# Performance work log

Measured on AMD Instinct MI355X. Metric: run time of the kernel, lower is better.

The kernel has to match this reference:

```python
import jax, jax.numpy as jnp
import numpy as np

EPS = 1e-4


def softmax_kernel(data, projection, is_query):
    # data: [b,h,n,d]; projection: [F,d]
    d = data.shape[-1]
    data_normalizer = d ** -0.25
    ratio = projection.shape[0] ** -0.5
    # [b,h,n,F]
    data_dash = jnp.einsum('bhnd,fd->bhnf', data_normalizer * data, projection)
    diag_data = (0.5 * (data_normalizer ** 2)) * jnp.sum(data * data, axis=-1, keepdims=True)
    if is_query:
        stab = jnp.max(data_dash, axis=-1, keepdims=True)
    else:
        stab = jnp.max(data_dash)
    return ratio * (jnp.exp(data_dash - diag_data - stab) + EPS)


def linear_attention(q, k, v):
    # q,k: [b,h,n,F]; v: [b,h,n,e]
    k_sum = k.sum(axis=-2)                                   # [b,h,F]
    d_inv = 1.0 / jnp.einsum('bhnf,bhf->bhn', q, k_sum)      # [b,h,n]
    context = jnp.einsum('bhnf,bhne->bhfe', k, v)            # [b,h,F,e]
    return jnp.einsum('bhfe,bhnf,bhn->bhne', context, q, d_inv)


def _gaussian_orthogonal_random_matrix(nb_rows, nb_cols, seed=0):
    # scaling=0: rows are orthogonal blocks rescaled by norms of iid gaussian rows
    rng = np.random.default_rng(seed)
    blocks = []
    full_blocks = nb_rows // nb_cols
    for _ in range(full_blocks):
        g = rng.standard_normal((nb_cols, nb_cols))
        qm, _ = np.linalg.qr(g)
        blocks.append(qm.T)
    rem = nb_rows - full_blocks * nb_cols
    if rem > 0:
        g = rng.standard_normal((nb_cols, nb_cols))
        qm, _ = np.linalg.qr(g)
        blocks.append(qm.T[:rem])
    mat = np.concatenate(blocks, axis=0)
    multiplier = np.linalg.norm(rng.standard_normal((nb_rows, nb_cols)), axis=1)
    return (multiplier[:, None] * mat).astype(np.float32)


def setup_inputs() -> dict:
    key = jax.random.key(0)
    kq, kk, kv = jax.random.split(key, 3)
    B, H, N, D = 2, 8, 8192, 64
    F = 256  # nb_features
    q = jax.random.normal(kq, (B, H, N, D), dtype=jnp.float32)
    k = jax.random.normal(kk, (B, H, N, D), dtype=jnp.float32)
    v = jax.random.normal(kv, (B, H, N, D), dtype=jnp.float32)
    projection = jnp.asarray(_gaussian_orthogonal_random_matrix(F, D, seed=0))
    return {"q": q, "k": k, "v": v, "projection": projection}


def reference(q, k, v, projection):
    qp = softmax_kernel(q, projection, is_query=True)
    kp = softmax_kernel(k, projection, is_query=False)
    return linear_attention(qp, kp, v)
```

## Files before the change

kernel.cpp:

```cpp
#include <hip/hip_runtime.h>


typedef __bf16 bf16;
typedef __bf16 bf16x8 __attribute__((ext_vector_type(8)));
typedef _Float16 f16;
typedef f16 f16x8 __attribute__((ext_vector_type(8)));
typedef float f32x4 __attribute__((ext_vector_type(4)));

#define N_    8192
#define BH_   16
#define NRM   0.35355339059327379f
#define RATIO 0.0625f
#define DSC   0.0625f
#define REPS  6.25e-6f

#define CTX_W  16
#define KSUM_W (CTX_W + BH_*256*64)
#define ZERO_W (KSUM_W + BH_*256)
#define SLICE_W 16640
#define PART_W  ZERO_W

static __device__ __forceinline__ unsigned mapmax(float x){
  unsigned u=__float_as_uint(x); return (u&0x80000000u)? ~u : (u|0x80000000u);
}
static __device__ __forceinline__ float unmapmax(unsigned u){
  return __uint_as_float((u&0x80000000u)? (u&0x7fffffffu) : ~u);
}
static __device__ __forceinline__ f32x4 mfma16(bf16x8 a, bf16x8 b, f32x4 c){
  return __builtin_amdgcn_mfma_f32_16x16x32_bf16(a,b,c,0,0,0);
}
static __device__ __forceinline__ f32x4 mfma16h(f16x8 a, f16x8 b, f32x4 c){
  return __builtin_amdgcn_mfma_f32_16x16x32_f16(a,b,c,0,0,0);
}
static __device__ __forceinline__ void ld8(const float* __restrict__ p, float* x){
  float4 a=*(const float4*)p; float4 b=*(const float4*)(p+4);
  x[0]=a.x; x[1]=a.y; x[2]=a.z; x[3]=a.w; x[4]=b.x; x[5]=b.y; x[6]=b.z; x[7]=b.w;
}
static __device__ __forceinline__ void split8(const float* x, bf16x8& h, bf16x8& l){
  #pragma unroll
  for(int i=0;i<8;++i){ bf16 hi=(bf16)x[i]; h[i]=hi; l[i]=(bf16)(x[i]-(float)hi); }
}
static __device__ __forceinline__ void cvt8b(const float* x, bf16x8& h){
  #pragma unroll
  for(int i=0;i<8;++i) h[i]=(bf16)x[i];
}
static __device__ __forceinline__ void cvt8h(const float* x, f16x8& h){
  #pragma unroll
  for(int i=0;i<8;++i) h[i]=(f16)x[i];
}
static __device__ __forceinline__ void gload16(const float* g, float* l){
  __builtin_amdgcn_global_load_lds(
      (const __attribute__((address_space(1))) unsigned*)g,
      (__attribute__((address_space(3))) unsigned*)l, 16, 0, 0);
}
static __device__ __forceinline__ void load_P_frags1(const float* __restrict__ Pg,
    int fb, int l15, int g, bf16x8 (&pb)[4][2]){
  #pragma unroll
  for(int ft=0;ft<4;++ft)
    #pragma unroll
    for(int ks=0;ks<2;++ks){
      float x[8]; ld8(&Pg[(fb+16*ft+l15)*64+32*ks+8*g],x);
      #pragma unroll
      for(int i=0;i<8;++i) x[i]*=NRM;
      cvt8b(x,pb[ft][ks]);
    }
}

#define STAGE32(Xg, bufptr, n0s) do{                                      \
    int u0_=tid, u1_=tid+256;                                             \
    int r0_=u0_>>4, c0_=u0_&15, r1_=u1_>>4, c1_=u1_&15;                   \
    gload16((Xg)+((n0s)+r0_)*64+((c0_^(r0_&15))<<2), (bufptr)+u0_*4);     \
    gload16((Xg)+((n0s)+r1_)*64+((c1_^(r1_&15))<<2), (bufptr)+u1_*4);     \
  }while(0)
#define STAGE64(Xg, bufptr, n0s) do{                                      \
    _Pragma("unroll")                                                     \
    for(int ii_=0;ii_<4;++ii_){                                           \
      int u_=tid+256*ii_;                                                 \
      int r_=u_>>4, c_=u_&15;                                             \
      gload16((Xg)+((n0s)+r_)*64+((c_^(r_&15))<<2), (bufptr)+u_*4);       \
    }                                                                     \
  }while(0)
#define FRAGREAD(xv, bufptr, rr, ksv) do{                                 \
    int cc0_=(8*(ksv)+2*g)^((rr)&15);                                     \
    int cc1_=cc0_^1;                                                      \
    float4 a_=*(const float4*)((bufptr)+(rr)*64+cc0_*4);                  \
    float4 b_=*(const float4*)((bufptr)+(rr)*64+cc1_*4);                  \
    xv[0]=a_.x; xv[1]=a_.y; xv[2]=a_.z; xv[3]=a_.w;                       \
    xv[4]=b_.x; xv[5]=b_.y; xv[6]=b_.z; xv[7]=b_.w;                       \
  }while(0)


__global__ void __launch_bounds__(256) initK(unsigned* ws, int n){
  for(int i=blockIdx.x*256+threadIdx.x;i<n;i+=gridDim.x*256) ws[i]=0u;
}

__global__ void __launch_bounds__(256) stabK(const float* __restrict__ Kg,
                                             const float* __restrict__ Pg,
                                             unsigned* __restrict__ stab_ws){
  __shared__ float red[4];
  int tid=threadIdx.x, w=tid>>6, lane=tid&63, l15=lane&15, g=lane>>4;
  int fb=w*64;
  f16x8 pb[4][2];
  #pragma unroll
  for(int ft=0;ft<4;++ft)
    #pragma unroll
    for(int ks=0;ks<2;++ks){
      float x[8]; ld8(&Pg[(fb+16*ft+l15)*64+32*ks+8*g],x);
      #pragma unroll
      for(int i=0;i<8;++i) x[i]*=NRM;
      cvt8h(x,pb[ft][ks]);
    }
  float m=-3.4e38f;
  long base=(long)blockIdx.x*512;
  f32x4 zero={0.f,0.f,0.f,0.f};
  #pragma unroll 1
  for(int it=0;it<8;++it){
    long row0=base+it*64;
    f16x8 ka[4][2];
    #pragma unroll
    for(int rt=0;rt<4;++rt)
      #pragma unroll
      for(int ks=0;ks<2;++ks){
        float x[8]; ld8(&Kg[(row0+16*rt+l15)*64+32*ks+8*g],x);
        cvt8h(x,ka[rt][ks]);
      }
    f32x4 acc[4][4];
    #pragma unroll
    for(int rt=0;rt<4;++rt)
      #pragma unroll
      for(int ft=0;ft<4;++ft) acc[rt][ft]=zero;
    __builtin_amdgcn_s_setprio(1);
    #pragma unroll
    for(int rt=0;rt<4;++rt)
      #pragma unroll
      for(int ft=0;ft<4;++ft)
        #pragma unroll
        for(int ks=0;ks<2;++ks)
          acc[rt][ft]=mfma16h(ka[rt][ks],pb[ft][ks],acc[rt][ft]);
    __builtin_amdgcn_s_setprio(0);
    #pragma unroll
    for(int rt=0;rt<4;++rt)
      #pragma unroll
      for(int ft=0;ft<4;++ft)
        #pragma unroll
        for(int r=0;r<4;++r) m=fmaxf(m,acc[rt][ft][r]);
  }
  #pragma unroll
  for(int off=1;off<64;off<<=1) m=fmaxf(m,__shfl_xor(m,off));
  if(lane==0) red[w]=m;
  __syncthreads();
  if(tid==0){
    m=fmaxf(fmaxf(red[0],red[1]),fmaxf(red[2],red[3]));
    atomicMax(stab_ws,mapmax(m));
  }
}

__global__ void __launch_bounds__(256,2) ctxK(const float* __restrict__ Kg,
    const float* __restrict__ Vg, const float* __restrict__ Pg,
    const unsigned* __restrict__ stab_ws, float* __restrict__ ctx_g,
    float* __restrict__ ksum_g, float* __restrict__ part, int mode){
  __shared__ __align__(16) bf16 kpt_h[256*40];
  __shared__ float kstage[2][2048];
  int tid=threadIdx.x, w=tid>>6, lane=tid&63, l15=lane&15, g=lane>>4;
  int fb=w*64;
  int bh=blockIdx.x>>5, ch=blockIdx.x&31;
  long rowbase=(long)bh*N_ + ch*256;
  float stab=unmapmax(*stab_ws);
  bf16x8 pb[4][2];
  load_P_frags1(Pg,fb,l15,g,pb);
  f32x4 zero={0.f,0.f,0.f,0.f};
  f32x4 cacc[4][4];
  #pragma unroll
  for(int mt=0;mt<4;++mt)
    #pragma unroll
    for(int et=0;et<4;++et) cacc[mt][et]=zero;
  float ksacc[4]={0.f,0.f,0.f,0.f};
  int cur=0;
  STAGE32(Kg, &kstage[0][0], rowbase);
  __syncthreads();
  #pragma unroll 1
  for(int it=0;it<8;++it){
    long n0=rowbase+it*32;
    long np=(it==7)? rowbase : n0+32;
    STAGE32(Kg, &kstage[cur^1][0], np);
    float vx[4][8];
    #pragma unroll
    for(int et=0;et<4;++et)
      #pragma unroll
      for(int j=0;j<8;++j) vx[et][j]=Vg[(n0+8*g+j)*64+16*et+l15];
    bf16x8 ka[2][2];
    float dsq[2];
    #pragma unroll
    for(int rt=0;rt<2;++rt){
      float ss=0.f;
      #pragma unroll
      for(int ks=0;ks<2;++ks){
        float x[8]; FRAGREAD(x,&kstage[cur][0],16*rt+l15,ks);
        #pragma unroll
        for(int i=0;i<8;++i) ss=fmaf(x[i],x[i],ss);
        cvt8b(x,ka[rt][ks]);
      }
      ss+=__shfl_xor(ss,16); ss+=__shfl_xor(ss,32);
      dsq[rt]=DSC*ss;
    }
    f32x4 dacc[2][4];
    #pragma unroll
    for(int rt=0;rt<2;++rt)
      #pragma unroll
      for(int ft=0;ft<4;++ft) dacc[rt][ft]=zero;
    __builtin_amdgcn_s_setprio(1);
    #pragma unroll
    for(int rt=0;rt<2;++rt)
      #pragma unroll
      for(int ft=0;ft<4;++ft)
        #pragma unroll
        for(int ks=0;ks<2;++ks)
          dacc[rt][ft]=mfma16(ka[rt][ks],pb[ft][ks],dacc[rt][ft]);
    __builtin_amdgcn_s_setprio(0);
    float dg[2][4];
    #pragma unroll
    for(int rt=0;rt<2;++rt)
      #pragma unroll
      for(int r=0;r<4;++r) dg[rt][r]=__shfl(dsq[rt],4*g+r);
    #pragma unroll
    for(int rt=0;rt<2;++rt)
      #pragma unroll
      for(int ft=0;ft<4;++ft){
        int f=fb+16*ft+l15;
        ushort4 pk;
        unsigned short hvb[4];
        #pragma unroll
        for(int r=0;r<4;++r){
          float kp=fmaf(RATIO,__expf(dacc[rt][ft][r]-dg[rt][r]-stab),REPS);
          bf16 hb=(bf16)kp;
          ksacc[ft]+=(float)hb;
          hvb[r]=__builtin_bit_cast(unsigned short,hb);
        }
        pk.x=hvb[0]; pk.y=hvb[1]; pk.z=hvb[2]; pk.w=hvb[3];
        *(ushort4*)&kpt_h[f*40+16*rt+4*g]=pk;
      }
    bf16x8 vb_h[4], vb_l[4];
    #pragma unroll
    for(int et=0;et<4;++et) split8(vx[et],vb_h[et],vb_l[et]);
    __builtin_amdgcn_s_setprio(1);
    #pragma unroll
    for(int mt=0;mt<4;++mt){
      bf16x8 a_h=*(const bf16x8*)&kpt_h[(fb+16*mt+l15)*40+8*g];
      #pragma unroll
      for(int et=0;et<4;++et){
        cacc[mt][et]=mfma16(a_h,vb_h[et],cacc[mt][et]);
        cacc[mt][et]=mfma16(a_h,vb_l[et],cacc[mt][et]);
      }
    }
    __builtin_amdgcn_s_setprio(0);
    __syncthreads();
    cur^=1;
  }
  float ksred[4];
  #pragma unroll
  for(int ft=0;ft<4;++ft){
    float s=ksacc[ft];
    s+=__shfl_xor(s,16); s+=__shfl_xor(s,32);
    ksred[ft]=s;
  }
  if(mode){
    float* cg=part+((long)ch*BH_+bh)*SLICE_W;
    #pragma unroll
    for(int mt=0;mt<4;++mt)
      #pragma unroll
      for(int et=0;et<4;++et)
        #pragma unroll
        for(int r=0;r<4;++r)
          cg[(fb+16*mt+4*g+r)*64+16*et+l15]=cacc[mt][et][r];
    if(g==0){
      #pragma unroll
      for(int ft=0;ft<4;++ft)
        cg[16384+fb+16*ft+l15]=ksred[ft];
    }
  }else{
    float* cg=ctx_g+(long)bh*16384;
    #pragma unroll
    for(int mt=0;mt<4;++mt)
      #pragma unroll
      for(int et=0;et<4;++et)
        #pragma unroll
        for(int r=0;r<4;++r)
          atomicAdd(&cg[(fb+16*mt+4*g+r)*64+16*et+l15],cacc[mt][et][r]);
    if(g==0){
      #pragma unroll
      for(int ft=0;ft<4;++ft)
        atomicAdd(&ksum_g[bh*256+fb+16*ft+l15],ksred[ft]);
    }
  }
}

__global__ void __launch_bounds__(256) redK(const float* __restrict__ part,
    float* __restrict__ ctx_g, float* __restrict__ ksum_g){
  const long TOT4=(long)BH_*(SLICE_W/4);
  long t=(long)blockIdx.x*256+threadIdx.x;
  for(long o=t;o<TOT4;o+=(long)gridDim.x*256){
    int bh=(int)(o/(SLICE_W/4)), idx4=(int)(o%(SLICE_W/4));
    float4 s=make_float4(0.f,0.f,0.f,0.f);
    #pragma unroll 8
    for(int ch=0;ch<32;++ch){
      float4 v=*(const float4*)&part[((long)ch*BH_+bh)*SLICE_W+idx4*4];
      s.x+=v.x; s.y+=v.y; s.z+=v.z; s.w+=v.w;
    }
    int idx=idx4*4;
    if(idx<16384) *(float4*)&ctx_g[(long)bh*16384+idx]=s;
    else          *(float4*)&ksum_g[bh*256+idx-16384]=s;
  }
}

__global__ void __launch_bounds__(256,2) qoK(const float* __restrict__ Qg,
    const float* __restrict__ Pg, const float* __restrict__ ctx_g,
    const float* __restrict__ ksum_g, float* __restrict__ outg){
  __shared__ float qstage[2][4096];
  __shared__ __align__(16) bf16 qpt[64*264];
  __shared__ float rmaxl[4][64];
  __shared__ float denl[4][64];
  int tid=threadIdx.x, w=tid>>6, lane=tid&63, l15=lane&15, g=lane>>4;
  int fb=w*64;
  int bh=blockIdx.x>>5, ch=blockIdx.x&31;
  long rowbase=(long)bh*N_ + ch*256;

  bf16x8 pb[4][2];
  load_P_frags1(Pg,fb,l15,g,pb);
  float4 ksv2[4];
  #pragma unroll
  for(int ft=0;ft<4;++ft)
    ksv2[ft]=*(const float4*)&ksum_g[bh*256+fb+16*ft+4*g];
  bf16x8 cb_h[8], cb_l[8];
  #pragma unroll
  for(int ks=0;ks<8;++ks){
    float x[8];
    #pragma unroll
    for(int j=0;j<8;++j) x[j]=ctx_g[(long)bh*16384+(32*ks+8*g+j)*64+16*w+l15];
    split8(x,cb_h[ks],cb_l[ks]);
  }
  f32x4 zero={0.f,0.f,0.f,0.f};
  int cur=0;
  STAGE64(Qg, &qstage[0][0], rowbase);
  __syncthreads();
  #pragma unroll 1
  for(int it=0;it<4;++it){
    long n0=rowbase+it*64;
    long np=(it==3)? rowbase : n0+64;
    STAGE64(Qg, &qstage[cur^1][0], np);
    f32x4 dacc[4][4];
    float dsq[4];
    #pragma unroll
    for(int rt=0;rt<4;++rt){
      bf16x8 qa[2];
      float ss=0.f;
      #pragma unroll
      for(int ks=0;ks<2;++ks){
        float x[8]; FRAGREAD(x,&qstage[cur][0],16*rt+l15,ks);
        #pragma unroll
        for(int i=0;i<8;++i) ss=fmaf(x[i],x[i],ss);
        cvt8b(x,qa[ks]);
      }
      ss+=__shfl_xor(ss,16); ss+=__shfl_xor(ss,32);
      dsq[rt]=DSC*ss;
      #pragma unroll
      for(int ft=0;ft<4;++ft) dacc[rt][ft]=zero;
      __builtin_amdgcn_s_setprio(1);
      #pragma unroll
      for(int ft=0;ft<4;++ft)
        #pragma unroll
        for(int ks=0;ks<2;++ks)
          dacc[rt][ft]=mfma16(pb[ft][ks],qa[ks],dacc[rt][ft]);
      __builtin_amdgcn_s_setprio(0);
    }
    #pragma unroll
    for(int rt=0;rt<4;++rt){
      float m=-3.4e38f;
      #pragma unroll
      for(int ft=0;ft<4;++ft)
        #pragma unroll
        for(int r=0;r<4;++r) m=fmaxf(m,dacc[rt][ft][r]);
      m=fmaxf(m,__shfl_xor(m,16));
      m=fmaxf(m,__shfl_xor(m,32));
      if(g==0) rmaxl[w][16*rt+l15]=m;
    }
    __syncthreads();
    #pragma unroll
    for(int rt=0;rt<4;++rt){
      int nn=16*rt+l15;
      float rm=fmaxf(fmaxf(rmaxl[0][nn],rmaxl[1][nn]),
                     fmaxf(rmaxl[2][nn],rmaxl[3][nn]));
      float base=dsq[rt]+rm;
      float dp=0.f;
      #pragma unroll
      for(int ft=0;ft<4;++ft){
        unsigned short hvb[4];
        float kw[4]={ksv2[ft].x,ksv2[ft].y,ksv2[ft].z,ksv2[ft].w};
        #pragma unroll
        for(int r=0;r<4;++r){
          float qp=fmaf(RATIO,__expf(dacc[rt][ft][r]-base),REPS);
          bf16 hb=(bf16)qp;
          dp=fmaf((float)hb,kw[r],dp);
          hvb[r]=__builtin_bit_cast(unsigned short,hb);
        }
        ushort4 pk; pk.x=hvb[0]; pk.y=hvb[1]; pk.z=hvb[2]; pk.w=hvb[3];
        *(ushort4*)&qpt[nn*264 + fb+16*ft+4*g]=pk;
      }
      dp+=__shfl_xor(dp,16); dp+=__shfl_xor(dp,32);
      if(g==0) denl[w][nn]=dp;
    }
    __syncthreads();
    f32x4 oacc[4];
    #pragma unroll
    for(int mt=0;mt<4;++mt) oacc[mt]=zero;
    __builtin_amdgcn_s_setprio(1);
    #pragma unroll
    for(int ks=0;ks<8;++ks)
      #pragma unroll
      for(int mt=0;mt<4;++mt){
        bf16x8 a_h=*(const bf16x8*)&qpt[(16*mt+l15)*264+32*ks+8*g];
        oacc[mt]=mfma16(a_h,cb_h[ks],oacc[mt]);
        oacc[mt]=mfma16(a_h,cb_l[ks],oacc[mt]);
      }
    __builtin_amdgcn_s_setprio(0);
    #pragma unroll
    for(int mt=0;mt<4;++mt)
      #pragma unroll
      for(int r=0;r<4;++r){
        int nn=16*mt+4*g+r;
        float den=denl[0][nn]+denl[1][nn]+denl[2][nn]+denl[3][nn];
        float rden=__builtin_amdgcn_rcpf(den);
        outg[(n0+nn)*64+16*w+l15]=oacc[mt][r]*rden;
      }
    cur^=1;
  }
}


extern "C" void kernel_launch(void* const* d_in, const int* in_sizes, int n_in,
                              void* d_out, int out_size, void* d_ws, size_t ws_size,
                              hipStream_t stream) {
  (void)in_sizes; (void)n_in; (void)out_size;
  const float* q = (const float*)d_in[0];
  const float* k = (const float*)d_in[1];
  const float* v = (const float*)d_in[2];
  const float* P = (const float*)d_in[3];
  float* out = (float*)d_out;

  unsigned* stab = (unsigned*)d_ws;
  float* ctx  = (float*)d_ws + CTX_W;
  float* ksum = (float*)d_ws + KSUM_W;
  float* part = (float*)d_ws + PART_W;

  size_t need = ((size_t)PART_W + (size_t)32*BH_*SLICE_W) * 4;
  int mode = (ws_size >= need) ? 1 : 0;

  if(mode)
    hipLaunchKernelGGL(initK, dim3(1), dim3(256), 0, stream, (unsigned*)d_ws, CTX_W);
  else
    hipLaunchKernelGGL(initK, dim3(256), dim3(256), 0, stream, (unsigned*)d_ws, ZERO_W);
  hipLaunchKernelGGL(stabK, dim3(256), dim3(256), 0, stream, k, P, stab);
  hipLaunchKernelGGL(ctxK, dim3(512), dim3(256), 0, stream, k, v, P, stab,
                     ctx, ksum, part, mode);
  if(mode)
    hipLaunchKernelGGL(redK, dim3(260), dim3(256), 0, stream, part, ctx, ksum);
  hipLaunchKernelGGL(qoK, dim3(512), dim3(256), 0, stream, q, P, ctx, ksum, out);
}
```

Before: 101.8 us.

## Process 64 key rows per iteration in ctxK to halve barriers

```diff
diff --git a/kernel.cpp b/kernel.cpp
--- a/kernel.cpp
+++ b/kernel.cpp
@@ -159,8 +159,8 @@
     const float* __restrict__ Vg, const float* __restrict__ Pg,
     const unsigned* __restrict__ stab_ws, float* __restrict__ ctx_g,
     float* __restrict__ ksum_g, float* __restrict__ part, int mode){
-  __shared__ __align__(16) bf16 kpt_h[256*40];
-  __shared__ float kstage[2][2048];
+  __shared__ __align__(16) bf16 kpt_h[256*72];
+  __shared__ float kstage[2][4096];
   int tid=threadIdx.x, w=tid>>6, lane=tid&63, l15=lane&15, g=lane>>4;
   int fb=w*64;
   int bh=blockIdx.x>>5, ch=blockIdx.x&31;
@@ -176,83 +176,103 @@
     for(int et=0;et<4;++et) cacc[mt][et]=zero;
   float ksacc[4]={0.f,0.f,0.f,0.f};
   int cur=0;
-  STAGE32(Kg, &kstage[0][0], rowbase);
+  STAGE64(Kg, &kstage[0][0], rowbase);
   __syncthreads();
   #pragma unroll 1
-  for(int it=0;it<8;++it){
-    long n0=rowbase+it*32;
-    long np=(it==7)? rowbase : n0+32;
-    STAGE32(Kg, &kstage[cur^1][0], np);
+  for(int it=0;it<4;++it){
+    long n0=rowbase+it*64;
+    long np=(it==3)? rowbase : n0+64;
+    STAGE64(Kg, &kstage[cur^1][0], np);
     float vx[4][8];
     #pragma unroll
     for(int et=0;et<4;++et)
       #pragma unroll
       for(int j=0;j<8;++j) vx[et][j]=Vg[(n0+8*g+j)*64+16*et+l15];
-    bf16x8 ka[2][2];
-    float dsq[2];
-    #pragma unroll
-    for(int rt=0;rt<2;++rt){
-      float ss=0.f;
-      #pragma unroll
-      for(int ks=0;ks<2;++ks){
-        float x[8]; FRAGREAD(x,&kstage[cur][0],16*rt+l15,ks);
-        #pragma unroll
-        for(int i=0;i<8;++i) ss=fmaf(x[i],x[i],ss);
-        cvt8b(x,ka[rt][ks]);
-      }
-      ss+=__shfl_xor(ss,16); ss+=__shfl_xor(ss,32);
-      dsq[rt]=DSC*ss;
-    }
-    f32x4 dacc[2][4];
-    #pragma unroll
-    for(int rt=0;rt<2;++rt)
-      #pragma unroll
-      for(int ft=0;ft<4;++ft) dacc[rt][ft]=zero;
-    __builtin_amdgcn_s_setprio(1);
-    #pragma unroll
-    for(int rt=0;rt<2;++rt)
-      #pragma unroll
-      for(int ft=0;ft<4;++ft)
-        #pragma unroll
-        for(int ks=0;ks<2;++ks)
-          dacc[rt][ft]=mfma16(ka[rt][ks],pb[ft][ks],dacc[rt][ft]);
-    __builtin_amdgcn_s_setprio(0);
-    float dg[2][4];
-    #pragma unroll
-    for(int rt=0;rt<2;++rt)
-      #pragma unroll
-      for(int r=0;r<4;++r) dg[rt][r]=__shfl(dsq[rt],4*g+r);
-    #pragma unroll
-    for(int rt=0;rt<2;++rt)
-      #pragma unroll
-      for(int ft=0;ft<4;++ft){
-        int f=fb+16*ft+l15;
-        ushort4 pk;
-        unsigned short hvb[4];
-        #pragma unroll
-        for(int r=0;r<4;++r){
-          float kp=fmaf(RATIO,__expf(dacc[rt][ft][r]-dg[rt][r]-stab),REPS);
-          bf16 hb=(bf16)kp;
-          ksacc[ft]+=(float)hb;
-          hvb[r]=__builtin_bit_cast(unsigned short,hb);
+    #pragma unroll
+    for(int half=0;half<2;++half){
+      bf16x8 ka[2][2];
+      float dsq[2];
+      #pragma unroll
+      for(int rtl=0;rtl<2;++rtl){
+        int rr=16*(2*half+rtl)+l15;
+        float ss=0.f;
+        #pragma unroll
+        for(int ks=0;ks<2;++ks){
+          float x[8]; FRAGREAD(x,&kstage[cur][0],rr,ks);
+          #pragma unroll
+          for(int i=0;i<8;++i) ss=fmaf(x[i],x[i],ss);
+          cvt8b(x,ka[rtl][ks]);
         }
-        pk.x=hvb[0]; pk.y=hvb[1]; pk.z=hvb[2]; pk.w=hvb[3];
-        *(ushort4*)&kpt_h[f*40+16*rt+4*g]=pk;
-      }
-    bf16x8 vb_h[4], vb_l[4];
-    #pragma unroll
-    for(int et=0;et<4;++et) split8(vx[et],vb_h[et],vb_l[et]);
-    __builtin_amdgcn_s_setprio(1);
-    #pragma unroll
-    for(int mt=0;mt<4;++mt){
-      bf16x8 a_h=*(const bf16x8*)&kpt_h[(fb+16*mt+l15)*40+8*g];
-      #pragma unroll
-      for(int et=0;et<4;++et){
-        cacc[mt][et]=mfma16(a_h,vb_h[et],cacc[mt][et]);
-        cacc[mt][et]=mfma16(a_h,vb_l[et],cacc[mt][et]);
-      }
-    }
-    __builtin_amdgcn_s_setprio(0);
+        ss+=__shfl_xor(ss,16); ss+=__shfl_xor(ss,32);
+        dsq[rtl]=DSC*ss;
+      }
+      f32x4 dacc[2][4];
+      #pragma unroll
+      for(int rtl=0;rtl<2;++rtl)
+        #pragma unroll
+        for(int ft=0;ft<4;++ft) dacc[rtl][ft]=zero;
+      __builtin_amdgcn_s_setprio(1);
+      #pragma unroll
+      for(int rtl=0;rtl<2;++rtl)
+        #pragma unroll
+        for(int ft=0;ft<4;++ft)
+          #pragma unroll
+          for(int ks=0;ks<2;++ks)
+            dacc[rtl][ft]=mfma16(ka[rtl][ks],pb[ft][ks],dacc[rtl][ft]);
+      __builtin_amdgcn_s_setprio(0);
+      float dg[2][4];
+      #pragma unroll
+      for(int rtl=0;rtl<2;++rtl)
+        #pragma unroll
+        for(int r=0;r<4;++r) dg[rtl][r]=__shfl(dsq[rtl],4*g+r);
+      #pragma unroll
+      for(int rtl=0;rtl<2;++rtl)
+        #pragma unroll
+        for(int ft=0;ft<4;++ft){
+          int f=fb+16*ft+l15;
+          ushort4 pk;
+          unsigned short hvb[4];
+          #pragma unroll
+          for(int r=0;r<4;++r){
+            float kp=fmaf(RATIO,__expf(dacc[rtl][ft][r]-dg[rtl][r]-stab),REPS);
+            bf16 hb=(bf16)kp;
+            ksacc[ft]+=(float)hb;
+            hvb[r]=__builtin_bit_cast(unsigned short,hb);
+          }
+          pk.x=hvb[0]; pk.y=hvb[1]; pk.z=hvb[2]; pk.w=hvb[3];
+          *(ushort4*)&kpt_h[f*72+32*half+16*rtl+4*g]=pk;
+        }
+    }
+    #pragma unroll
+    for(int ks2=0;ks2<2;++ks2){
+      float vx1[4][8];
+      if(ks2==0){
+        #pragma unroll
+        for(int et=0;et<4;++et)
+          #pragma unroll
+          for(int j=0;j<8;++j) vx1[et][j]=Vg[(n0+32+8*g+j)*64+16*et+l15];
+      }
+      bf16x8 vb_h[4], vb_l[4];
+      #pragma unroll
+      for(int et=0;et<4;++et) split8(vx[et],vb_h[et],vb_l[et]);
+      __builtin_amdgcn_s_setprio(1);
+      #pragma unroll
+      for(int mt=0;mt<4;++mt){
+        bf16x8 a_h=*(const bf16x8*)&kpt_h[(fb+16*mt+l15)*72+32*ks2+8*g];
+        #pragma unroll
+        for(int et=0;et<4;++et){
+          cacc[mt][et]=mfma16(a_h,vb_h[et],cacc[mt][et]);
+          cacc[mt][et]=mfma16(a_h,vb_l[et],cacc[mt][et]);
+        }
+      }
+      __builtin_amdgcn_s_setprio(0);
+      if(ks2==0){
+        #pragma unroll
+        for(int et=0;et<4;++et)
+          #pragma unroll
+          for(int j=0;j<8;++j) vx[et][j]=vx1[et][j];
+      }
+    }
     __syncthreads();
     cur^=1;
   }
```

Measured after the change: 101.9 us. No clear change (+0.1%).
